# Performance work log

Measured on AMD Instinct MI355X. Metric: run time of the kernel, lower is better.

Reference implementation:

```python
import jax, jax.numpy as jnp
import numpy as np

K = 5
BN_EPS = 1e-5


def _knn(xyz1, xyz2, embedding_lens):
    # squared pairwise distances [B, N, S]
    d2 = (jnp.sum(xyz1 ** 2, -1)[:, :, None]
          + jnp.sum(xyz2 ** 2, -1)[:, None, :]
          - 2.0 * jnp.einsum('bnc,bsc->bns', xyz1, xyz2))
    S = xyz2.shape[1]
    valid2 = jnp.arange(S)[None, :] < embedding_lens[:, None]  # [B, S]
    d2 = jnp.where(valid2[:, None, :], d2, jnp.float32(1e10))
    neg, idx = jax.lax.top_k(-d2, K)  # K smallest distances
    return -neg, idx  # squared dists [B,N,K], indices [B,N,K]


def _masked_bn(x, mask_f, gamma, beta):
    # x: [B, N, C]; mask_f: [B, N, 1] float; stats over valid positions only
    cnt = jnp.sum(mask_f)
    mean = jnp.sum(x * mask_f, axis=(0, 1)) / cnt
    var = jnp.sum(((x - mean) ** 2) * mask_f, axis=(0, 1)) / cnt
    return (x - mean) * jax.lax.rsqrt(var + BN_EPS) * gamma + beta


def setup_inputs() -> dict:
    key = jax.random.key(0)
    ks = jax.random.split(key, 8)
    B, N, S, D1, D2 = 16, 2048, 512, 384, 384
    xyz1 = jax.random.normal(ks[0], (B, N, 3), jnp.float32)
    xyz2 = jax.random.normal(ks[1], (B, S, 3), jnp.float32)
    points1 = jax.random.normal(ks[2], (B, N, D1), jnp.float32)
    points2 = jax.random.normal(ks[3], (B, S, D2), jnp.float32)
    point_lens = jax.random.randint(ks[4], (B,), N // 2, N + 1).astype(jnp.int32)
    embedding_lens = jax.random.randint(ks[5], (B,), S // 2, S + 1).astype(jnp.int32)
    point_mask = jnp.arange(N)[None, :] < point_lens[:, None]  # [B, N] bool
    Cin = D1 + D2
    W0 = jax.random.normal(ks[6], (768, Cin), jnp.float32) * (1.0 / np.sqrt(Cin))
    W1 = jax.random.normal(ks[7], (384, 768), jnp.float32) * (1.0 / np.sqrt(768))
    return dict(xyz1=xyz1, xyz2=xyz2, points1=points1, points2=points2,
                point_lens=point_lens, embedding_lens=embedding_lens,
                point_mask=point_mask,
                W0=W0, g0=jnp.ones((768,), jnp.float32), b0=jnp.zeros((768,), jnp.float32),
                W1=W1, g1=jnp.ones((384,), jnp.float32), b1=jnp.zeros((384,), jnp.float32))


def reference(xyz1, xyz2, points1, points2, point_lens, embedding_lens,
              point_mask, W0, g0, b0, W1, g1, b1):
    B, N, _ = xyz1.shape
    D2 = points2.shape[-1]
    dists, idx = _knn(xyz1[..., :3], xyz2, embedding_lens)
    eps = jnp.finfo(dists.dtype).eps
    dist_recip = 1.0 / (dists + eps)                    # [B, N, K]
    weight = dist_recip / jnp.sum(dist_recip, axis=2, keepdims=True)
    # masked gather: points2[b, idx[b,n,k], :] -> [B, N, K, D2]
    gathered = jnp.take_along_axis(points2, idx.reshape(B, N * K)[..., None],
                                   axis=1).reshape(B, N, K, D2)
    interp = jnp.sum(gathered * weight[..., None], axis=2)  # [B, N, D2]
    x = jnp.concatenate([points1, interp], axis=-1)          # [B, N, D1+D2]
    mask_f = point_mask.astype(x.dtype)[..., None]           # [B, N, 1]
    for W, g, b in ((W0, g0, b0), (W1, g1, b1)):
        x = jnp.einsum('bnc,dc->bnd', x, W)  # 1x1 conv, no bias
        x = jax.nn.relu(_masked_bn(x, mask_f, g, b))
    return x
```

## Files before the change

kernel.cpp:

```cpp
#include <hip/hip_runtime.h>
#include <cstdint>
#include <cstddef>

typedef unsigned short u16;
typedef __bf16 bf16x8 __attribute__((ext_vector_type(8)));
typedef float    f32x4 __attribute__((ext_vector_type(4)));
typedef unsigned int u32x4 __attribute__((ext_vector_type(4)));
typedef unsigned short u16x4 __attribute__((ext_vector_type(4)));

constexpr int BB   = 16;
constexpr int NN   = 2048;
constexpr int SS   = 512;
constexpr int DD   = 384;
constexpr int CIN  = 768;
constexpr int HID  = 768;
constexpr int OUTC = 384;
constexpr int MROWS = BB * NN;
constexpr float KNN_EPS = 1.1920929e-07f;
constexpr float BN_EPS  = 1e-5f;

constexpr size_t OFF_W0B  = 0;
constexpr size_t OFF_W1B  = OFF_W0B  + (size_t)HID*CIN*2;
constexpr size_t OFF_IDX  = OFF_W1B  + (size_t)OUTC*HID*2;
constexpr size_t OFF_WGT  = OFF_IDX  + (size_t)MROWS*5*4;
constexpr size_t OFF_SUM1 = OFF_WGT  + (size_t)MROWS*5*4;
constexpr size_t OFF_SUM2 = OFF_SUM1 + (size_t)HID*2*4;
constexpr size_t OFF_XCAT = OFF_SUM2 + (size_t)OUTC*2*4;
constexpr size_t OFF_H1   = OFF_XCAT + (size_t)MROWS*CIN*2;
constexpr size_t OFF_P2B  = OFF_H1   + (size_t)MROWS*HID*2;
constexpr size_t NEED_P2B = OFF_P2B  + (size_t)BB*SS*DD*2;

__device__ inline float bf2f(u16 u){ unsigned int i = ((unsigned int)u)<<16; float f; __builtin_memcpy(&f,&i,4); return f; }
__device__ inline u16 f2bf(float f){ unsigned int x; __builtin_memcpy(&x,&f,4);
  unsigned int r = (x + 0x7fffu + ((x>>16)&1u)) >> 16; return (u16)r; }

__device__ inline void async16(const void* g, void* l){
  __builtin_amdgcn_global_load_lds((const __attribute__((address_space(1))) void*)g,
                                   (__attribute__((address_space(3))) void*)l, 16, 0, 0);
}

__global__ void cvtw_kernel(const float* __restrict__ W0, const float* __restrict__ W1,
                            const float* __restrict__ p2,
                            u16* __restrict__ W0b, u16* __restrict__ W1b,
                            u16* __restrict__ p2b, float* __restrict__ sums){
  int t = blockIdx.x*256 + threadIdx.x;
  if (t < HID*CIN)  W0b[t] = f2bf(W0[t]);
  if (t < OUTC*HID) W1b[t] = f2bf(W1[t]);
  if (p2b != nullptr && t < BB*SS*DD) p2b[t] = f2bf(p2[t]);
  if (t < (HID + OUTC)*2) sums[t] = 0.f;
}

__global__ __launch_bounds__(256) void knn_kernel(const float* __restrict__ xyz1,
                                                  const float* __restrict__ xyz2,
                                                  const int* __restrict__ elens,
                                                  int* __restrict__ idxO, float* __restrict__ wO){
  __shared__ f32x4 sp[SS];
  const int tid = threadIdx.x;
  const int wv = tid >> 6, lane = tid & 63;
  const int wg = blockIdx.x*4 + wv;
  const int b = wg >> 11;
  const int n = wg & (NN-1);
  for (int s = tid; s < SS; s += 256){
    float x = xyz2[((size_t)b*SS + s)*3 + 0];
    float y = xyz2[((size_t)b*SS + s)*3 + 1];
    float z = xyz2[((size_t)b*SS + s)*3 + 2];
    f32x4 v; v[0]=x; v[1]=y; v[2]=z; v[3]=x*x+y*y+z*z;
    sp[s]=v;
  }
  __syncthreads();
  const size_t qoff = ((size_t)b*NN + n)*3;
  const float qx = xyz1[qoff+0], qy = xyz1[qoff+1], qz = xyz1[qoff+2];
  const float qq = qx*qx + qy*qy + qz*qz;
  const int Sl = elens[b];

  float d0=1e30f,d1=1e30f,d2v=1e30f,d3=1e30f,d4=1e30f;
  int   i0=0,i1=0,i2=0,i3=0,i4=0;
  #pragma unroll
  for (int j=0;j<8;j++){
    const int s = lane + j*64;
    f32x4 v = sp[s];
    float d = (s < Sl) ? (qq + v[3] - 2.f*(qx*v[0] + qy*v[1] + qz*v[2])) : 1e30f;
    bool lt4=d<d4, lt3=d<d3, lt2=d<d2v, lt1=d<d1, lt0=d<d0;
    float nd4 = lt3 ? d3 : (lt4 ? d : d4); int ni4 = lt3 ? i3 : (lt4 ? s : i4);
    float nd3 = lt2 ? d2v: (lt3 ? d : d3); int ni3 = lt2 ? i2 : (lt3 ? s : i3);
    float nd2 = lt1 ? d1 : (lt2 ? d : d2v);int ni2 = lt1 ? i1 : (lt2 ? s : i2);
    float nd1 = lt0 ? d0 : (lt1 ? d : d1); int ni1 = lt0 ? i0 : (lt1 ? s : i1);
    float nd0 = lt0 ? d  : d0;             int ni0 = lt0 ? s  : i0;
    d4=nd4;i4=ni4; d3=nd3;i3=ni3; d2v=nd2;i2=ni2; d1=nd1;i1=ni1; d0=nd0;i0=ni0;
  }
  float outd[5]; int outi[5];
  #pragma unroll
  for (int r=0;r<5;r++){
    float bd = d0; int bs = i0;
    #pragma unroll
    for (int m=1;m<64;m<<=1){
      float od = __shfl_xor(bd, m, 64);
      int   os = __shfl_xor(bs, m, 64);
      if (od < bd || (od == bd && os < bs)){ bd = od; bs = os; }
    }
    outd[r]=bd; outi[r]=bs;
    if (d0 == bd && i0 == bs){ d0=d1;i0=i1; d1=d2v;i1=i2; d2v=d3;i2=i3; d3=d4;i3=i4; d4=1e30f;i4=0; }
  }
  if (lane == 0){
    float r0=1.f/(outd[0]+KNN_EPS), r1=1.f/(outd[1]+KNN_EPS), r2=1.f/(outd[2]+KNN_EPS),
          r3=1.f/(outd[3]+KNN_EPS), r4=1.f/(outd[4]+KNN_EPS);
    float inv = 1.f/(r0+r1+r2+r3+r4);
    size_t base = (size_t)wg*5;
    idxO[base+0]=outi[0]; idxO[base+1]=outi[1]; idxO[base+2]=outi[2]; idxO[base+3]=outi[3]; idxO[base+4]=outi[4];
    wO[base+0]=r0*inv; wO[base+1]=r1*inv; wO[base+2]=r2*inv; wO[base+3]=r3*inv; wO[base+4]=r4*inv;
  }
}

template<bool BF16G>
__global__ __launch_bounds__(384) void xcat_kernel(const float* __restrict__ p1,
                                                   const float* __restrict__ p2,
                                                   const u16* __restrict__ p2b,
                                                   const int* __restrict__ idx,
                                                   const float* __restrict__ wgt,
                                                   u16* __restrict__ xcat){
  const int t = threadIdx.x;
  const int rloc = t / 96, c4 = t % 96;
  const int row = blockIdx.x*4 + rloc;
  const int b = row >> 11;
  const int c = c4*4;
  f32x4 v1 = *reinterpret_cast<const f32x4*>(p1 + (size_t)row*DD + c);
  size_t ib = (size_t)row*5;
  f32x4 acc = {0.f,0.f,0.f,0.f};
  #pragma unroll
  for (int k=0;k<5;k++){
    int id = idx[ib+k]; float w = wgt[ib+k];
    if (BF16G){
      u16x4 g = *reinterpret_cast<const u16x4*>(p2b + ((size_t)b*SS + id)*DD + c);
      #pragma unroll
      for (int j=0;j<4;j++) acc[j] += w * bf2f(g[j]);
    } else {
      f32x4 g = *reinterpret_cast<const f32x4*>(p2 + ((size_t)b*SS + id)*DD + c);
      #pragma unroll
      for (int j=0;j<4;j++) acc[j] += w * g[j];
    }
  }
  u16x4 o1, o2;
  #pragma unroll
  for (int j=0;j<4;j++){ o1[j] = f2bf(v1[j]); o2[j] = f2bf(acc[j]); }
  *reinterpret_cast<u16x4*>(xcat + (size_t)row*CIN + c)      = o1;
  *reinterpret_cast<u16x4*>(xcat + (size_t)row*CIN + DD + c) = o2;
}

__global__ __launch_bounds__(512, 4) void gemm1_kernel(const u16* __restrict__ A,
                                                       const u16* __restrict__ Bw,
                                                       u16* __restrict__ Cout,
                                                       const int* __restrict__ plen,
                                                       float* __restrict__ sums){
  constexpr int K   = CIN;
  constexpr int NC  = HID;
  constexpr int GX  = NC/128;
  constexpr int NT  = K/64;
  constexpr int NWG = GX*256;
  constexpr int CPX = NWG/8;
  __shared__ u16 Ash[2][128*64];
  __shared__ u16 Bsh[2][128*64];
  const int tid  = threadIdx.x;
  const int lane = tid & 63, wv = tid >> 6;
  const int wr = wv >> 2, wc = wv & 3;
  const int l15 = lane & 15, l16 = lane >> 4;

  const int logical = (blockIdx.x & 7)*CPX + (blockIdx.x >> 3);
  const int bn = logical % GX, bm = logical / GX;

  int srowS[2]; int sk8S[2];
  #pragma unroll
  for (int j=0;j<2;j++){
    int ch = j*512 + tid;
    srowS[j] = ch >> 3;
    sk8S[j]  = (ch & 7) ^ ((ch >> 3) & 7);
  }
  const u16* gA0 = A  + (size_t)(bm*128 + srowS[0])*K + sk8S[0]*8;
  const u16* gA1 = A  + (size_t)(bm*128 + srowS[1])*K + sk8S[1]*8;
  const u16* gB0 = Bw + (size_t)(bn*128 + srowS[0])*K + sk8S[0]*8;
  const u16* gB1 = Bw + (size_t)(bn*128 + srowS[1])*K + sk8S[1]*8;
  const int dst0 = (wv*64)*16;
  const int dst1 = (512 + wv*64)*16;

  auto stageA = [&](int tt, int bi){
    async16(gA0 + tt*64, (char*)&Ash[bi][0] + dst0);
    async16(gA1 + tt*64, (char*)&Ash[bi][0] + dst1);
  };
  auto stageB = [&](int tt, int bi){
    async16(gB0 + tt*64, (char*)&Bsh[bi][0] + dst0);
    async16(gB1 + tt*64, (char*)&Bsh[bi][0] + dst1);
  };

  int aoff[4][2], boff[2][2];
  #pragma unroll
  for (int m=0;m<4;m++){
    int r = wr*64 + m*16 + l15;
    #pragma unroll
    for (int kh=0;kh<2;kh++)
      aoff[m][kh] = (r*8 + (((kh*4 + l16) ^ (r & 7)))) * 8;
  }
  #pragma unroll
  for (int n=0;n<2;n++){
    int r = wc*32 + n*16 + l15;
    #pragma unroll
    for (int kh=0;kh<2;kh++)
      boff[n][kh] = (r*8 + (((kh*4 + l16) ^ (r & 7)))) * 8;
  }

  f32x4 acc[4][2] = {};

  stageA(0,0); stageB(0,0); stageA(1,1); stageB(1,1);
  asm volatile("s_waitcnt vmcnt(4)" ::: "memory");
  __builtin_amdgcn_s_barrier();
  __builtin_amdgcn_sched_barrier(0);

  for (int t=0; t<NT; ++t){
    const int cur = t & 1;
    const int tt = (t+2 < NT) ? (t+2) : (NT-1);
    bf16x8 af[4][2];
    #pragma unroll
    for (int m=0;m<4;m++){
      af[m][0] = *reinterpret_cast<const bf16x8*>(&Ash[cur][aoff[m][0]]);
      af[m][1] = *reinterpret_cast<const bf16x8*>(&Ash[cur][aoff[m][1]]);
    }
    bf16x8 b00 = *reinterpret_cast<const bf16x8*>(&Bsh[cur][boff[0][0]]);
    bf16x8 b10 = *reinterpret_cast<const bf16x8*>(&Bsh[cur][boff[1][0]]);
    asm volatile("s_waitcnt lgkmcnt(0)" ::: "memory");
    __builtin_amdgcn_s_barrier();
    __builtin_amdgcn_sched_barrier(0);
    stageA(tt, cur);
    __builtin_amdgcn_s_setprio(1);
    acc[0][0] = __builtin_amdgcn_mfma_f32_16x16x32_bf16(af[0][0], b00, acc[0][0], 0,0,0);
    acc[1][0] = __builtin_amdgcn_mfma_f32_16x16x32_bf16(af[1][0], b00, acc[1][0], 0,0,0);
    acc[2][0] = __builtin_amdgcn_mfma_f32_16x16x32_bf16(af[2][0], b00, acc[2][0], 0,0,0);
    acc[3][0] = __builtin_amdgcn_mfma_f32_16x16x32_bf16(af[3][0], b00, acc[3][0], 0,0,0);
    acc[0][1] = __builtin_amdgcn_mfma_f32_16x16x32_bf16(af[0][0], b10, acc[0][1], 0,0,0);
    acc[1][1] = __builtin_amdgcn_mfma_f32_16x16x32_bf16(af[1][0], b10, acc[1][1], 0,0,0);
    acc[2][1] = __builtin_amdgcn_mfma_f32_16x16x32_bf16(af[2][0], b10, acc[2][1], 0,0,0);
    acc[3][1] = __builtin_amdgcn_mfma_f32_16x16x32_bf16(af[3][0], b10, acc[3][1], 0,0,0);
    __builtin_amdgcn_s_setprio(0);
    bf16x8 b01 = *reinterpret_cast<const bf16x8*>(&Bsh[cur][boff[0][1]]);
    bf16x8 b11 = *reinterpret_cast<const bf16x8*>(&Bsh[cur][boff[1][1]]);
    asm volatile("s_waitcnt lgkmcnt(0)" ::: "memory");
    __builtin_amdgcn_s_barrier();
    __builtin_amdgcn_sched_barrier(0);
    stageB(tt, cur);
    __builtin_amdgcn_s_setprio(1);
    acc[0][0] = __builtin_amdgcn_mfma_f32_16x16x32_bf16(af[0][1], b01, acc[0][0], 0,0,0);
    acc[1][0] = __builtin_amdgcn_mfma_f32_16x16x32_bf16(af[1][1], b01, acc[1][0], 0,0,0);
    acc[2][0] = __builtin_amdgcn_mfma_f32_16x16x32_bf16(af[2][1], b01, acc[2][0], 0,0,0);
    acc[3][0] = __builtin_amdgcn_mfma_f32_16x16x32_bf16(af[3][1], b01, acc[3][0], 0,0,0);
    acc[0][1] = __builtin_amdgcn_mfma_f32_16x16x32_bf16(af[0][1], b11, acc[0][1], 0,0,0);
    acc[1][1] = __builtin_amdgcn_mfma_f32_16x16x32_bf16(af[1][1], b11, acc[1][1], 0,0,0);
    acc[2][1] = __builtin_amdgcn_mfma_f32_16x16x32_bf16(af[2][1], b11, acc[2][1], 0,0,0);
    acc[3][1] = __builtin_amdgcn_mfma_f32_16x16x32_bf16(af[3][1], b11, acc[3][1], 0,0,0);
    __builtin_amdgcn_s_setprio(0);
    asm volatile("s_waitcnt vmcnt(4)" ::: "memory");
    __builtin_amdgcn_s_barrier();
    __builtin_amdgcn_sched_barrier(0);
  }
  asm volatile("s_waitcnt vmcnt(0)" ::: "memory");
  __syncthreads();

  #pragma unroll
  for (int m=0;m<4;m++){
    int r0 = bm*128 + wr*64 + m*16 + l16*4;
    #pragma unroll
    for (int n=0;n<2;n++){
      int c = bn*128 + wc*32 + n*16 + l15;
      #pragma unroll
      for (int r=0;r<4;r++)
        Cout[(size_t)(r0+r)*NC + c] = f2bf(acc[m][n][r]);
    }
  }

  const int pl = plen[bm >> 4];
  const int rbase = (bm & 15)*128 + wr*64 + l16*4;
  float cs[2] = {0.f,0.f}, cs2[2] = {0.f,0.f};
  #pragma unroll
  for (int m=0;m<4;m++){
    #pragma unroll
    for (int r=0;r<4;r++){
      if (rbase + m*16 + r < pl){
        #pragma unroll
        for (int n=0;n<2;n++){
          float v = acc[m][n][r];
          cs[n] += v; cs2[n] += v*v;
        }
      }
    }
  }
  #pragma unroll
  for (int n=0;n<2;n++){
    cs[n]  += __shfl_xor(cs[n], 16, 64);  cs[n]  += __shfl_xor(cs[n], 32, 64);
    cs2[n] += __shfl_xor(cs2[n], 16, 64); cs2[n] += __shfl_xor(cs2[n], 32, 64);
  }
  float* lsum = (float*)&Ash[0][0];
  if (tid < 256) lsum[tid] = 0.f;
  __syncthreads();
  if (l16 == 0){
    #pragma unroll
    for (int n=0;n<2;n++){
      int col = wc*32 + n*16 + l15;
      atomicAdd(&lsum[col], cs[n]);
      atomicAdd(&lsum[128 + col], cs2[n]);
    }
  }
  __syncthreads();
  if (tid < 128)       atomicAdd(&sums[bn*128 + tid], lsum[tid]);
  else if (tid < 256)  atomicAdd(&sums[NC + bn*128 + (tid-128)], lsum[tid]);
}

__global__ __launch_bounds__(256) void gemm2_kernel(const u16* __restrict__ A,
                                                    const u16* __restrict__ Bw,
                                                    u16* __restrict__ Yout,
                                                    const int* __restrict__ plen,
                                                    float* __restrict__ sums,
                                                    const float* __restrict__ sum1,
                                                    const float* __restrict__ g0,
                                                    const float* __restrict__ b0){
  constexpr int GX = 3;
  constexpr int K  = HID;
  constexpr int NC = GX*128;
  constexpr int NSTEP = K/32;
  constexpr int NWG = GX*256;
  constexpr int CPX = NWG/8;
  __shared__ u16 As[2][128*32];
  __shared__ u16 Bs[3][128*32];
  __shared__ float cfl[HID*2];
  const int tid  = threadIdx.x;
  const int lane = tid & 63, wv = tid >> 6;
  const int wr = wv >> 1, wc = wv & 1;
  const int l15 = lane & 15, l16 = lane >> 4;
  const int sw  = (l15 >> 1) & 3;

  const int logical = (blockIdx.x & 7)*CPX + (blockIdx.x >> 3);
  const int bn = logical % GX, bm = logical / GX;

  int c8S[2], ldso[2];
  const u16* Ab[2]; const u16* Bb[2];
  #pragma unroll
  for (int j=0;j<2;j++){
    int ch = j*256 + wv*64 + lane;
    int row = ch >> 2;
    int c8 = (ch & 3) ^ ((ch >> 3) & 3);
    c8S[j] = c8;
    ldso[j] = (j*256 + wv*64)*16;
    Ab[j] = A  + (size_t)(bm*128 + row)*K + c8*8;
    Bb[j] = Bw + (size_t)(bn*128 + row)*K + c8*8;
  }

  auto stageB = [&](int nb, int kt){
    #pragma unroll
    for (int j=0;j<2;j++) async16(Bb[j] + kt*32, (char*)&Bs[nb][0] + ldso[j]);
  };
  u32x4 hv0, hv1;
  auto loadA = [&](int kt){
    hv0 = *reinterpret_cast<const u32x4*>(Ab[0] + kt*32);
    hv1 = *reinterpret_cast<const u32x4*>(Ab[1] + kt*32);
  };
  auto bnwrite = [&](int nb, int kt){
    #pragma unroll
    for (int j=0;j<2;j++){
      const int k0 = kt*32 + c8S[j]*8;
      float av[8], bv[8];
      *reinterpret_cast<f32x4*>(av)   = *reinterpret_cast<const f32x4*>(cfl + k0);
      *reinterpret_cast<f32x4*>(av+4) = *reinterpret_cast<const f32x4*>(cfl + k0 + 4);
      *reinterpret_cast<f32x4*>(bv)   = *reinterpret_cast<const f32x4*>(cfl + K + k0);
      *reinterpret_cast<f32x4*>(bv+4) = *reinterpret_cast<const f32x4*>(cfl + K + k0 + 4);
      u32x4 v = j ? hv1 : hv0; u32x4 o;
      #pragma unroll
      for (int q=0;q<4;q++){
        float lo = bf2f((u16)(v[q] & 0xffffu));
        float hi = bf2f((u16)(v[q] >> 16));
        lo = fmaxf(lo*av[2*q]   + bv[2*q],   0.f);
        hi = fmaxf(hi*av[2*q+1] + bv[2*q+1], 0.f);
        o[q] = (unsigned int)f2bf(lo) | ((unsigned int)f2bf(hi) << 16);
      }
      *reinterpret_cast<u32x4*>((char*)&As[nb][0] + ldso[j] + lane*16) = o;
    }
  };

  f32x4 acc[4][4] = {};

  loadA(0);
  __builtin_amdgcn_sched_barrier(0);
  stageB(0, 0); stageB(1, 1);
  {
    float cnt = 0.f;
    #pragma unroll
    for (int b=0;b<BB;b++) cnt += (float)plen[b];
    const float icnt = 1.f / cnt;
    for (int c = tid; c < HID; c += 256){
      float mean = sum1[c] * icnt;
      float var  = fmaxf(sum1[HID + c]*icnt - mean*mean, 0.f);
      float a = g0[c] * rsqrtf(var + BN_EPS);
      cfl[c] = a;
      cfl[HID + c] = b0[c] - mean*a;
    }
  }
  __syncthreads();
  bnwrite(0, 0);
  asm volatile("s_waitcnt vmcnt(2) lgkmcnt(0)" ::: "memory");
  __builtin_amdgcn_s_barrier();

  int rb = 0, wb = 2;
  for (int kt=0; kt<NSTEP; ++kt){
    const bool pf1 = (kt+1 < NSTEP), pf2 = (kt+2 < NSTEP);
    if (pf1) loadA(kt+1);
    __builtin_amdgcn_sched_barrier(0);
    if (pf2) stageB(wb, kt+2);

    bf16x8 af[4], bfr[4];
    const int aslot = kt & 1;
    #pragma unroll
    for (int m=0;m<4;m++){
      int r = wr*64 + m*16 + l15;
      af[m] = *reinterpret_cast<const bf16x8*>(&As[aslot][r*32 + ((l16 ^ sw) << 3)]);
    }
    #pragma unroll
    for (int n=0;n<4;n++){
      int c = wc*64 + n*16 + l15;
      bfr[n] = *reinterpret_cast<const bf16x8*>(&Bs[rb][c*32 + ((l16 ^ sw) << 3)]);
    }
    #pragma unroll
    for (int m=0;m<4;m++)
      #pragma unroll
      for (int n=0;n<4;n++)
        acc[m][n] = __builtin_amdgcn_mfma_f32_16x16x32_bf16(af[m], bfr[n], acc[m][n], 0, 0, 0);

    if (pf1) bnwrite((kt+1)&1, kt+1);

    if (pf1){
      if (pf2) asm volatile("s_waitcnt vmcnt(2) lgkmcnt(0)" ::: "memory");
      else     asm volatile("s_waitcnt vmcnt(0) lgkmcnt(0)" ::: "memory");
      __builtin_amdgcn_s_barrier();
    }
    rb = (rb==2) ? 0 : rb+1;
    wb = (wb==2) ? 0 : wb+1;
  }

  #pragma unroll
  for (int m=0;m<4;m++){
    int r0 = bm*128 + wr*64 + m*16 + l16*4;
    #pragma unroll
    for (int n=0;n<4;n++){
      int c = bn*128 + wc*64 + n*16 + l15;
      #pragma unroll
      for (int r=0;r<4;r++)
        Yout[(size_t)(r0+r)*NC + c] = f2bf(acc[m][n][r]);
    }
  }

  const int pl = plen[bm >> 4];
  const int rbase = (bm & 15)*128 + wr*64 + l16*4;
  float cs[4] = {0.f,0.f,0.f,0.f}, cs2[4] = {0.f,0.f,0.f,0.f};
  #pragma unroll
  for (int m=0;m<4;m++){
    #pragma unroll
    for (int r=0;r<4;r++){
      if (rbase + m*16 + r < pl){
        #pragma unroll
        for (int n=0;n<4;n++){
          float v = acc[m][n][r];
          cs[n] += v; cs2[n] += v*v;
        }
      }
    }
  }
  #pragma unroll
  for (int n=0;n<4;n++){
    cs[n]  += __shfl_xor(cs[n], 16, 64);  cs[n]  += __shfl_xor(cs[n], 32, 64);
    cs2[n] += __shfl_xor(cs2[n], 16, 64); cs2[n] += __shfl_xor(cs2[n], 32, 64);
  }
  float* lsum = (float*)&As[0][0];
  lsum[tid] = 0.f;
  __syncthreads();
  if (l16 == 0){
    #pragma unroll
    for (int n=0;n<4;n++){
      int col = wc*64 + n*16 + l15;
      atomicAdd(&lsum[col], cs[n]);
      atomicAdd(&lsum[128 + col], cs2[n]);
    }
  }
  __syncthreads();
  if (tid < 128)       atomicAdd(&sums[bn*128 + tid], lsum[tid]);
  else                 atomicAdd(&sums[NC + bn*128 + (tid-128)], lsum[tid]);
}

__global__ __launch_bounds__(256) void final_kernel(const u16* __restrict__ Y,
                                                    float* __restrict__ O,
                                                    const float* __restrict__ sums,
                                                    const int* __restrict__ plen,
                                                    const float* __restrict__ g1,
                                                    const float* __restrict__ b1){
  __shared__ float cfl[OUTC*2];
  const int tid = threadIdx.x;
  {
    float cnt = 0.f;
    #pragma unroll
    for (int b=0;b<BB;b++) cnt += (float)plen[b];
    const float icnt = 1.f / cnt;
    for (int c = tid; c < OUTC; c += 256){
      float mean = sums[c] * icnt;
      float var  = fmaxf(sums[OUTC + c]*icnt - mean*mean, 0.f);
      float a = g1[c] * rsqrtf(var + BN_EPS);
      cfl[c] = a;
      cfl[OUTC + c] = b1[c] - mean*a;
    }
  }
  __syncthreads();
  const size_t base = (size_t)blockIdx.x * 128 * OUTC;
  for (int i = tid; i < 128*OUTC/8; i += 256){
    size_t f = base + (size_t)i*8;
    int c = (int)(f % (size_t)OUTC);
    u32x4 v = *reinterpret_cast<const u32x4*>(Y + f);
    f32x4 o0, o1;
    #pragma unroll
    for (int j=0;j<4;j++){
      float lo = bf2f((u16)(v[j] & 0xffffu));
      float hi = bf2f((u16)(v[j] >> 16));
      float r0 = fmaxf(lo*cfl[c+2*j]   + cfl[OUTC+c+2*j],   0.f);
      float r1 = fmaxf(hi*cfl[c+2*j+1] + cfl[OUTC+c+2*j+1], 0.f);
      if (j < 2){ o0[2*j] = r0; o0[2*j+1] = r1; }
      else      { o1[2*(j-2)] = r0; o1[2*(j-2)+1] = r1; }
    }
    *reinterpret_cast<f32x4*>(O + f)     = o0;
    *reinterpret_cast<f32x4*>(O + f + 4) = o1;
  }
}

extern "C" void kernel_launch(void* const* d_in, const int* in_sizes, int n_in,
                              void* d_out, int out_size, void* d_ws, size_t ws_size,
                              hipStream_t stream){
  (void)in_sizes; (void)n_in; (void)out_size;
  const float* xyz1 = (const float*)d_in[0];
  const float* xyz2 = (const float*)d_in[1];
  const float* p1   = (const float*)d_in[2];
  const float* p2   = (const float*)d_in[3];
  const int*   plen = (const int*)d_in[4];
  const int*   elen = (const int*)d_in[5];
  const float* W0   = (const float*)d_in[7];
  const float* g0   = (const float*)d_in[8];
  const float* b0   = (const float*)d_in[9];
  const float* W1   = (const float*)d_in[10];
  const float* g1   = (const float*)d_in[11];
  const float* b1   = (const float*)d_in[12];
  float* out = (float*)d_out;
  char*  ws  = (char*)d_ws;

  u16*   W0b  = (u16*)  (ws + OFF_W0B);
  u16*   W1b  = (u16*)  (ws + OFF_W1B);
  int*   idxb = (int*)  (ws + OFF_IDX);
  float* wgtb = (float*)(ws + OFF_WGT);
  float* sum1 = (float*)(ws + OFF_SUM1);
  float* sum2 = (float*)(ws + OFF_SUM2);
  u16*   xcat = (u16*)  (ws + OFF_XCAT);
  u16*   h1   = (u16*)  (ws + OFF_H1);
  const bool hasP2b = (ws_size >= NEED_P2B);
  u16*   p2b  = hasP2b ? (u16*)(ws + OFF_P2B) : nullptr;

  {
    int maxT = hasP2b ? (BB*SS*DD) : (HID*CIN);
    cvtw_kernel<<<(maxT + 255)/256, 256, 0, stream>>>(W0, W1, p2, W0b, W1b, p2b, sum1);
  }
  knn_kernel<<<MROWS/4, 256, 0, stream>>>(xyz1, xyz2, elen, idxb, wgtb);
  if (hasP2b) xcat_kernel<true ><<<MROWS/4, 384, 0, stream>>>(p1, p2, p2b, idxb, wgtb, xcat);
  else        xcat_kernel<false><<<MROWS/4, 384, 0, stream>>>(p1, p2, p2b, idxb, wgtb, xcat);

  gemm1_kernel<<<6*256, 512, 0, stream>>>(xcat, W0b, h1, plen, sum1);

  gemm2_kernel<<<3*256, 256, 0, stream>>>(h1, W1b, xcat , plen, sum2, sum1, g0, b0);

  final_kernel<<<MROWS/128, 256, 0, stream>>>(xcat , out, sum2, plen, g1, b1);
}
```

Before: 183.1 us.

## Restructure gemm2 to 512 threads with K=64 tiles and split-phase MFMA pipeline

Rewrites the second GEMM (with fused BN0+ReLU on the A operand) to use 8 waves per block, 64-wide K tiles with double-buffered LDS for A and B, and an XOR swizzle over 8 chunks. The inner loop is split into two half-K phases with barriers, setprio around MFMA bursts, and B prefetch issued mid-iteration, apparently mirroring the gemm1 structure. The aim is to halve the number of loop iterations and barriers and to raise occupancy and MFMA issue density. In exchange it adds more barriers per iteration, uses more LDS per block, and gives each wave a smaller per-wave tile (4x2).

```diff
diff --git a/kernel.cpp b/kernel.cpp
--- a/kernel.cpp
+++ b/kernel.cpp
@@ -310,7 +310,7 @@
   else if (tid < 256)  atomicAdd(&sums[NC + bn*128 + (tid-128)], lsum[tid]);
 }
 
-__global__ __launch_bounds__(256) void gemm2_kernel(const u16* __restrict__ A,
+__global__ __launch_bounds__(512) void gemm2_kernel(const u16* __restrict__ A,
                                                     const u16* __restrict__ Bw,
                                                     u16* __restrict__ Yout,
                                                     const int* __restrict__ plen,
@@ -318,50 +318,50 @@
                                                     const float* __restrict__ sum1,
                                                     const float* __restrict__ g0,
                                                     const float* __restrict__ b0){
-  constexpr int GX = 3;
-  constexpr int K  = HID;
-  constexpr int NC = GX*128;
-  constexpr int NSTEP = K/32;
-  constexpr int NWG = GX*256;
+  constexpr int K   = HID;
+  constexpr int NC  = OUTC;
+  constexpr int GX  = NC/128;
+  constexpr int NT  = K/64;
+  constexpr int NWG = (MROWS/128)*GX;
   constexpr int CPX = NWG/8;
-  __shared__ u16 As[2][128*32];
-  __shared__ u16 Bs[3][128*32];
+  __shared__ u16 Ash[2][128*64];
+  __shared__ u16 Bsh[2][128*64];
   __shared__ float cfl[HID*2];
   const int tid  = threadIdx.x;
   const int lane = tid & 63, wv = tid >> 6;
-  const int wr = wv >> 1, wc = wv & 1;
+  const int wr = wv >> 2, wc = wv & 3;
   const int l15 = lane & 15, l16 = lane >> 4;
-  const int sw  = (l15 >> 1) & 3;
 
   const int logical = (blockIdx.x & 7)*CPX + (blockIdx.x >> 3);
   const int bn = logical % GX, bm = logical / GX;
 
-  int c8S[2], ldso[2];
-  const u16* Ab[2]; const u16* Bb[2];
+  int srowS[2]; int sk8S[2];
   #pragma unroll
   for (int j=0;j<2;j++){
-    int ch = j*256 + wv*64 + lane;
-    int row = ch >> 2;
-    int c8 = (ch & 3) ^ ((ch >> 3) & 3);
-    c8S[j] = c8;
-    ldso[j] = (j*256 + wv*64)*16;
-    Ab[j] = A  + (size_t)(bm*128 + row)*K + c8*8;
-    Bb[j] = Bw + (size_t)(bn*128 + row)*K + c8*8;
-  }
-
-  auto stageB = [&](int nb, int kt){
-    #pragma unroll
-    for (int j=0;j<2;j++) async16(Bb[j] + kt*32, (char*)&Bs[nb][0] + ldso[j]);
+    int ch = j*512 + tid;
+    srowS[j] = ch >> 3;
+    sk8S[j]  = (ch & 7) ^ ((ch >> 3) & 7);
+  }
+  const u16* gA0 = A  + (size_t)(bm*128 + srowS[0])*K + sk8S[0]*8;
+  const u16* gA1 = A  + (size_t)(bm*128 + srowS[1])*K + sk8S[1]*8;
+  const u16* gB0 = Bw + (size_t)(bn*128 + srowS[0])*K + sk8S[0]*8;
+  const u16* gB1 = Bw + (size_t)(bn*128 + srowS[1])*K + sk8S[1]*8;
+  const int dst0 = (wv*64)*16;
+  const int dst1 = (512 + wv*64)*16;
+
+  auto stageB = [&](int tt, int bi){
+    async16(gB0 + tt*64, (char*)&Bsh[bi][0] + dst0);
+    async16(gB1 + tt*64, (char*)&Bsh[bi][0] + dst1);
   };
   u32x4 hv0, hv1;
-  auto loadA = [&](int kt){
-    hv0 = *reinterpret_cast<const u32x4*>(Ab[0] + kt*32);
-    hv1 = *reinterpret_cast<const u32x4*>(Ab[1] + kt*32);
+  auto loadA = [&](int tt){
+    hv0 = *reinterpret_cast<const u32x4*>(gA0 + tt*64);
+    hv1 = *reinterpret_cast<const u32x4*>(gA1 + tt*64);
   };
-  auto bnwrite = [&](int nb, int kt){
+  auto bnwrite = [&](int tt, int bi){
     #pragma unroll
     for (int j=0;j<2;j++){
-      const int k0 = kt*32 + c8S[j]*8;
+      const int k0 = tt*64 + sk8S[j]*8;
       float av[8], bv[8];
       *reinterpret_cast<f32x4*>(av)   = *reinterpret_cast<const f32x4*>(cfl + k0);
       *reinterpret_cast<f32x4*>(av+4) = *reinterpret_cast<const f32x4*>(cfl + k0 + 4);
@@ -376,11 +376,27 @@
         hi = fmaxf(hi*av[2*q+1] + bv[2*q+1], 0.f);
         o[q] = (unsigned int)f2bf(lo) | ((unsigned int)f2bf(hi) << 16);
       }
-      *reinterpret_cast<u32x4*>((char*)&As[nb][0] + ldso[j] + lane*16) = o;
+      *reinterpret_cast<u32x4*>((char*)&Ash[bi][0] + (j*512 + tid)*16) = o;
     }
   };
 
-  f32x4 acc[4][4] = {};
+  int aoff[4][2], boff[2][2];
+  #pragma unroll
+  for (int m=0;m<4;m++){
+    int r = wr*64 + m*16 + l15;
+    #pragma unroll
+    for (int kh=0;kh<2;kh++)
+      aoff[m][kh] = (r*8 + (((kh*4 + l16) ^ (r & 7)))) * 8;
+  }
+  #pragma unroll
+  for (int n=0;n<2;n++){
+    int r = wc*32 + n*16 + l15;
+    #pragma unroll
+    for (int kh=0;kh<2;kh++)
+      boff[n][kh] = (r*8 + (((kh*4 + l16) ^ (r & 7)))) * 8;
+  }
+
+  f32x4 acc[4][2] = {};
 
   loadA(0);
   __builtin_amdgcn_sched_barrier(0);
@@ -390,7 +406,7 @@
     #pragma unroll
     for (int b=0;b<BB;b++) cnt += (float)plen[b];
     const float icnt = 1.f / cnt;
-    for (int c = tid; c < HID; c += 256){
+    for (int c = tid; c < HID; c += 512){
       float mean = sum1[c] * icnt;
       float var  = fmaxf(sum1[HID + c]*icnt - mean*mean, 0.f);
       float a = g0[c] * rsqrtf(var + BN_EPS);
@@ -402,49 +418,64 @@
   bnwrite(0, 0);
   asm volatile("s_waitcnt vmcnt(2) lgkmcnt(0)" ::: "memory");
   __builtin_amdgcn_s_barrier();
-
-  int rb = 0, wb = 2;
-  for (int kt=0; kt<NSTEP; ++kt){
-    const bool pf1 = (kt+1 < NSTEP), pf2 = (kt+2 < NSTEP);
-    if (pf1) loadA(kt+1);
+  __builtin_amdgcn_sched_barrier(0);
+
+  for (int t=0; t<NT; ++t){
+    const int cur = t & 1, nxt = cur ^ 1;
+    const bool pf1 = (t+1 < NT), pf2 = (t+2 < NT);
+    if (pf1) loadA(t+1);
     __builtin_amdgcn_sched_barrier(0);
-    if (pf2) stageB(wb, kt+2);
-
-    bf16x8 af[4], bfr[4];
-    const int aslot = kt & 1;
+    bf16x8 af[4][2];
     #pragma unroll
     for (int m=0;m<4;m++){
-      int r = wr*64 + m*16 + l15;
-      af[m] = *reinterpret_cast<const bf16x8*>(&As[aslot][r*32 + ((l16 ^ sw) << 3)]);
-    }
-    #pragma unroll
-    for (int n=0;n<4;n++){
-      int c = wc*64 + n*16 + l15;
-      bfr[n] = *reinterpret_cast<const bf16x8*>(&Bs[rb][c*32 + ((l16 ^ sw) << 3)]);
-    }
-    #pragma unroll
-    for (int m=0;m<4;m++)
-      #pragma unroll
-      for (int n=0;n<4;n++)
-        acc[m][n] = __builtin_amdgcn_mfma_f32_16x16x32_bf16(af[m], bfr[n], acc[m][n], 0, 0, 0);
-
-    if (pf1) bnwrite((kt+1)&1, kt+1);
-
-    if (pf1){
-      if (pf2) asm volatile("s_waitcnt vmcnt(2) lgkmcnt(0)" ::: "memory");
-      else     asm volatile("s_waitcnt vmcnt(0) lgkmcnt(0)" ::: "memory");
-      __builtin_amdgcn_s_barrier();
-    }
-    rb = (rb==2) ? 0 : rb+1;
-    wb = (wb==2) ? 0 : wb+1;
-  }
+      af[m][0] = *reinterpret_cast<const bf16x8*>(&Ash[cur][aoff[m][0]]);
+      af[m][1] = *reinterpret_cast<const bf16x8*>(&Ash[cur][aoff[m][1]]);
+    }
+    bf16x8 b00 = *reinterpret_cast<const bf16x8*>(&Bsh[cur][boff[0][0]]);
+    bf16x8 b10 = *reinterpret_cast<const bf16x8*>(&Bsh[cur][boff[1][0]]);
+    asm volatile("s_waitcnt lgkmcnt(0)" ::: "memory");
+    __builtin_amdgcn_s_barrier();
+    __builtin_amdgcn_sched_barrier(0);
+    __builtin_amdgcn_s_setprio(1);
+    acc[0][0] = __builtin_amdgcn_mfma_f32_16x16x32_bf16(af[0][0], b00, acc[0][0], 0,0,0);
+    acc[1][0] = __builtin_amdgcn_mfma_f32_16x16x32_bf16(af[1][0], b00, acc[1][0], 0,0,0);
+    acc[2][0] = __builtin_amdgcn_mfma_f32_16x16x32_bf16(af[2][0], b00, acc[2][0], 0,0,0);
+    acc[3][0] = __builtin_amdgcn_mfma_f32_16x16x32_bf16(af[3][0], b00, acc[3][0], 0,0,0);
+    acc[0][1] = __builtin_amdgcn_mfma_f32_16x16x32_bf16(af[0][0], b10, acc[0][1], 0,0,0);
+    acc[1][1] = __builtin_amdgcn_mfma_f32_16x16x32_bf16(af[1][0], b10, acc[1][1], 0,0,0);
+    acc[2][1] = __builtin_amdgcn_mfma_f32_16x16x32_bf16(af[2][0], b10, acc[2][1], 0,0,0);
+    acc[3][1] = __builtin_amdgcn_mfma_f32_16x16x32_bf16(af[3][0], b10, acc[3][1], 0,0,0);
+    __builtin_amdgcn_s_setprio(0);
+    bf16x8 b01 = *reinterpret_cast<const bf16x8*>(&Bsh[cur][boff[0][1]]);
+    bf16x8 b11 = *reinterpret_cast<const bf16x8*>(&Bsh[cur][boff[1][1]]);
+    asm volatile("s_waitcnt lgkmcnt(0)" ::: "memory");
+    __builtin_amdgcn_s_barrier();
+    __builtin_amdgcn_sched_barrier(0);
+    if (pf2) stageB(t+2, cur);
+    __builtin_amdgcn_s_setprio(1);
+    acc[0][0] = __builtin_amdgcn_mfma_f32_16x16x32_bf16(af[0][1], b01, acc[0][0], 0,0,0);
+    acc[1][0] = __builtin_amdgcn_mfma_f32_16x16x32_bf16(af[1][1], b01, acc[1][0], 0,0,0);
+    acc[2][0] = __builtin_amdgcn_mfma_f32_16x16x32_bf16(af[2][1], b01, acc[2][0], 0,0,0);
+    acc[3][0] = __builtin_amdgcn_mfma_f32_16x16x32_bf16(af[3][1], b01, acc[3][0], 0,0,0);
+    acc[0][1] = __builtin_amdgcn_mfma_f32_16x16x32_bf16(af[0][1], b11, acc[0][1], 0,0,0);
+    acc[1][1] = __builtin_amdgcn_mfma_f32_16x16x32_bf16(af[1][1], b11, acc[1][1], 0,0,0);
+    acc[2][1] = __builtin_amdgcn_mfma_f32_16x16x32_bf16(af[2][1], b11, acc[2][1], 0,0,0);
+    acc[3][1] = __builtin_amdgcn_mfma_f32_16x16x32_bf16(af[3][1], b11, acc[3][1], 0,0,0);
+    __builtin_amdgcn_s_setprio(0);
+    if (pf1) bnwrite(t+1, nxt);
+    if (pf2) asm volatile("s_waitcnt vmcnt(2) lgkmcnt(0)" ::: "memory");
+    else     asm volatile("s_waitcnt vmcnt(0) lgkmcnt(0)" ::: "memory");
+    __builtin_amdgcn_s_barrier();
+    __builtin_amdgcn_sched_barrier(0);
+  }
+  __syncthreads();
 
   #pragma unroll
   for (int m=0;m<4;m++){
     int r0 = bm*128 + wr*64 + m*16 + l16*4;
     #pragma unroll
-    for (int n=0;n<4;n++){
-      int c = bn*128 + wc*64 + n*16 + l15;
+    for (int n=0;n<2;n++){
+      int c = bn*128 + wc*32 + n*16 + l15;
       #pragma unroll
       for (int r=0;r<4;r++)
         Yout[(size_t)(r0+r)*NC + c] = f2bf(acc[m][n][r]);
@@ -453,14 +484,14 @@
 
   const int pl = plen[bm >> 4];
   const int rbase = (bm & 15)*128 + wr*64 + l16*4;
-  float cs[4] = {0.f,0.f,0.f,0.f}, cs2[4] = {0.f,0.f,0.f,0.f};
+  float cs[2] = {0.f,0.f}, cs2[2] = {0.f,0.f};
   #pragma unroll
   for (int m=0;m<4;m++){
     #pragma unroll
     for (int r=0;r<4;r++){
       if (rbase + m*16 + r < pl){
         #pragma unroll
-        for (int n=0;n<4;n++){
+        for (int n=0;n<2;n++){
           float v = acc[m][n][r];
           cs[n] += v; cs2[n] += v*v;
         }
@@ -468,24 +499,24 @@
     }
   }
   #pragma unroll
-  for (int n=0;n<4;n++){
+  for (int n=0;n<2;n++){
     cs[n]  += __shfl_xor(cs[n], 16, 64);  cs[n]  += __shfl_xor(cs[n], 32, 64);
     cs2[n] += __shfl_xor(cs2[n], 16, 64); cs2[n] += __shfl_xor(cs2[n], 32, 64);
   }
-  float* lsum = (float*)&As[0][0];
-  lsum[tid] = 0.f;
+  float* lsum = (float*)&Ash[0][0];
+  if (tid < 256) lsum[tid] = 0.f;
   __syncthreads();
   if (l16 == 0){
     #pragma unroll
-    for (int n=0;n<4;n++){
-      int col = wc*64 + n*16 + l15;
+    for (int n=0;n<2;n++){
+      int col = wc*32 + n*16 + l15;
       atomicAdd(&lsum[col], cs[n]);
       atomicAdd(&lsum[128 + col], cs2[n]);
     }
   }
   __syncthreads();
   if (tid < 128)       atomicAdd(&sums[bn*128 + tid], lsum[tid]);
-  else                 atomicAdd(&sums[NC + bn*128 + (tid-128)], lsum[tid]);
+  else if (tid < 256)  atomicAdd(&sums[NC + bn*128 + (tid-128)], lsum[tid]);
 }
 
 __global__ __launch_bounds__(256) void final_kernel(const u16* __restrict__ Y,
@@ -570,7 +601,7 @@
 
   gemm1_kernel<<<6*256, 512, 0, stream>>>(xcat, W0b, h1, plen, sum1);
 
-  gemm2_kernel<<<3*256, 256, 0, stream>>>(h1, W1b, xcat , plen, sum2, sum1, g0, b0);
+  gemm2_kernel<<<3*256, 512, 0, stream>>>(h1, W1b, xcat , plen, sum2, sum1, g0, b0);
 
   final_kernel<<<MROWS/128, 256, 0, stream>>>(xcat , out, sum2, plen, g1, b1);
 }
```

Result: faster. 172.7 us (median of 2 runs) (-5.7%).
